# Performance work log

Measured on AMD Instinct MI355X. Metric: run time of the kernel, lower is better.

## Reference

```python
import jax, jax.numpy as jnp
import numpy as np

LN_EPS = 1e-5
NEG_SLOPE = 0.2
INF = float((1 << 32) - 1)


def _ln(x, g, b):
    m = x.mean(-1, keepdims=True)
    v = ((x - m) ** 2).mean(-1, keepdims=True)
    return (x - m) * jax.lax.rsqrt(v + LN_EPS) * g + b


def setup_inputs() -> dict:
    B, M, NPG = 128, 256, 192      # graphs, max nodes per graph, actual nodes per graph
    N = B * NPG                    # 24576 total nodes
    E = N * 16                     # 393216 edges (avg degree 16)
    d, H, Od = 256, 4, 64          # input/attn dim, heads, per-head dim
    out_dim = 256
    key = jax.random.key(0)
    ks = jax.random.split(key, 24)
    s = 0.05
    p = lambda k, sh: jax.random.normal(k, sh, jnp.float32) * s

    node_feat = jax.random.normal(ks[0], (N, d), jnp.float32)
    edge_feat = jax.random.normal(ks[1], (E, d), jnp.float32)
    edge_index = jax.random.randint(ks[2], (2, E), 0, N)
    ptr = jnp.arange(B + 1, dtype=jnp.int32) * NPG
    row_valid = jnp.arange(M) < NPG
    attn_mask = jnp.broadcast_to(row_valid[None, :, None] & row_valid[None, None, :], (B, M, M))

    return dict(
        node_feat=node_feat, attn_mask=attn_mask, edge_feat=edge_feat,
        edge_index=edge_index, num_nodes=N, ptr=ptr,
        Wq=p(ks[3], (d, H * Od)), Wk=p(ks[4], (d, H * Od)), Wv=p(ks[5], (d, H * Od)),
        alphaQ=p(ks[6], (H, Od)), alphaK=p(ks[7], (H, Od)), attn_bias=p(ks[8], (H, Od)),
        gin_eps=jnp.zeros((), jnp.float32),
        gin_W1=p(ks[9], (d, 2 * d)), gin_b1=jnp.zeros((2 * d,), jnp.float32),
        gin_W2=p(ks[10], (2 * d, d)), gin_b2=jnp.zeros((d,), jnp.float32),
        ln1_g=jnp.ones((d,), jnp.float32), ln1_b=jnp.zeros((d,), jnp.float32),
        ln2_g=jnp.ones((d,), jnp.float32), ln2_b=jnp.zeros((d,), jnp.float32),
        ff_W1=p(ks[11], (2 * d, out_dim)), ff_b1=jnp.zeros((out_dim,), jnp.float32),
        ff_W2=p(ks[12], (out_dim, out_dim)), ff_b2=jnp.zeros((out_dim,), jnp.float32),
    )


def reference(node_feat, attn_mask, edge_feat, edge_index, num_nodes, ptr,
              Wq, Wk, Wv, alphaQ, alphaK, attn_bias,
              gin_eps, gin_W1, gin_b1, gin_W2, gin_b2,
              ln1_g, ln1_b, ln2_g, ln2_b,
              ff_W1, ff_b1, ff_W2, ff_b2):
    B, M = attn_mask.shape[:2]
    N, d = node_feat.shape
    H = alphaQ.shape[0]

    # graph -> dense batch layout (scatter by (graph, local position))
    node_ids = jnp.arange(N)
    batch_id = jnp.searchsorted(ptr, node_ids, side='right') - 1
    local = node_ids - ptr[batch_id]
    attn_input = jnp.zeros((B, M, d), node_feat.dtype).at[batch_id, local].set(node_feat)

    # GAT-style additive multi-head attention
    Qp = (attn_input @ Wq).reshape(B, M, H, -1)
    Kp = (attn_input @ Wk).reshape(B, M, H, -1)
    Vp = (attn_input @ Wv).reshape(B, M, H, -1)
    aQ = jnp.einsum('bmhd,hd->bmh', Qp, alphaQ)
    aK = jnp.einsum('bmhd,hd->bmh', Kp, alphaK)
    w = jax.nn.leaky_relu(aQ[:, :, None, :] + aK[:, None, :, :], NEG_SLOPE)  # [B,Q,K,H]
    w = jnp.where(attn_mask[..., None], w, -INF)
    w = jax.nn.softmax(w, axis=2)
    attn_out = (jnp.einsum('bqkh,bkhd->bqhd', w, Vp) + attn_bias).reshape(B, M, -1)

    attn_res = _ln(attn_out + attn_input, ln1_g, ln1_b)[batch_id, local]  # back to [N, d]

    # GIN conv: relu(x[dst] + e) scatter-summed to src, then 2-layer MLP
    msg = jax.nn.relu(node_feat[edge_index[1]] + edge_feat)
    agg = jax.ops.segment_sum(msg, edge_index[0], num_segments=num_nodes)
    h = (1.0 + gin_eps) * node_feat + agg
    gin = jax.nn.relu(h @ gin_W1 + gin_b1) @ gin_W2 + gin_b2
    gin_res = _ln(gin + node_feat, ln2_g, ln2_b)

    x = jnp.concatenate([gin_res, attn_res], axis=-1)  # [N, 2d]
    return jax.nn.relu(x @ ff_W1 + ff_b1) @ ff_W2 + ff_b2
```

## Files before the change

### kernel.cpp

```cpp
#include <hip/hip_runtime.h>

#define LN_EPS 1e-5f
#define NEG_SLOPE 0.2f

typedef __attribute__((ext_vector_type(8))) short short8;
typedef __attribute__((ext_vector_type(4))) float f32x4;

__device__ __forceinline__ unsigned short f2bf(float f) {
  union { float f; unsigned int u; } v;
  v.f = f;
  unsigned int r = v.u + 0x7fffu + ((v.u >> 16) & 1u);
  return (unsigned short)(r >> 16);
}
__device__ __forceinline__ float bf2f(unsigned short u) {
  union { unsigned int u; float f; } v;
  v.u = ((unsigned int)u) << 16;
  return v.f;
}

__device__ __forceinline__ void gld_lds16(const void* g, void* l) {
  __builtin_amdgcn_global_load_lds(
      (const __attribute__((address_space(1))) unsigned int*)g,
      (__attribute__((address_space(3))) unsigned int*)l, 16, 0, 0);
}

template <bool RELU, bool BIAS, bool OUTBF>
__device__ __forceinline__ void gemm_role(
    int t, char* smemc, const unsigned short* __restrict__ A,
    const unsigned short* __restrict__ Bt, const float* __restrict__ bias,
    void* __restrict__ Cv, int N, int K) {
  uint4* As = (uint4*)smemc;
  uint4* Bs = (uint4*)smemc + 512;
  const int tid = threadIdx.x;
  const int wid = tid >> 6, lane = tid & 63;
  const int nC = N >> 7;
  const int row0 = (t / nC) << 6;
  const int col0 = (t % nC) << 7;
  const int wr = wid >> 1, wc = wid & 1;
  const int fr = lane & 15, fq = lane >> 4;

  f32x4 acc[2][4];
#pragma unroll
  for (int m = 0; m < 2; ++m)
#pragma unroll
    for (int n = 0; n < 4; ++n) acc[m][n] = (f32x4){0.f, 0.f, 0.f, 0.f};

  for (int k0 = 0; k0 < K; k0 += 64) {
    __syncthreads();
#pragma unroll
    for (int c = 0; c < 2; ++c) {
      int idx = c * 256 + tid;
      int row = idx >> 3, gs = (idx & 7) ^ (row & 7);
      gld_lds16(A + (size_t)(row0 + row) * K + k0 + gs * 8, As + (idx & ~63));
    }
#pragma unroll
    for (int c = 0; c < 4; ++c) {
      int idx = c * 256 + tid;
      int row = idx >> 3, gs = (idx & 7) ^ (row & 7);
      gld_lds16(Bt + (size_t)(col0 + row) * K + k0 + gs * 8, Bs + (idx & ~63));
    }
    __syncthreads();
#pragma unroll
    for (int kk = 0; kk < 2; ++kk) {
      short8 af[2], bfr[4];
#pragma unroll
      for (int m = 0; m < 2; ++m) {
        int row = wr * 32 + m * 16 + fr;
        af[m] = *(const short8*)&As[row * 8 + ((kk * 4 + fq) ^ (row & 7))];
      }
#pragma unroll
      for (int n = 0; n < 4; ++n) {
        int col = wc * 64 + n * 16 + fr;
        bfr[n] = *(const short8*)&Bs[col * 8 + ((kk * 4 + fq) ^ (col & 7))];
      }
#pragma unroll
      for (int m = 0; m < 2; ++m)
#pragma unroll
        for (int n = 0; n < 4; ++n)
          acc[m][n] = __builtin_amdgcn_mfma_f32_16x16x32_bf16(af[m], bfr[n],
                                                              acc[m][n], 0, 0, 0);
    }
  }

#pragma unroll
  for (int n = 0; n < 4; ++n) {
    const int col = col0 + wc * 64 + n * 16 + fr;
    const float bv = BIAS ? bias[col] : 0.f;
#pragma unroll
    for (int m = 0; m < 2; ++m) {
#pragma unroll
      for (int r = 0; r < 4; ++r) {
        int row = row0 + wr * 32 + m * 16 + fq * 4 + r;
        float v = acc[m][n][r];
        if (BIAS) v += bv;
        if (RELU) v = fmaxf(v, 0.f);
        if (OUTBF)
          ((unsigned short*)Cv)[(size_t)row * N + col] = f2bf(v);
        else
          ((float*)Cv)[(size_t)row * N + col] = v;
      }
    }
  }
}

__device__ __forceinline__ void gather_role(
    int t, const float* __restrict__ node, const unsigned short* __restrict__ nf16,
    const float* __restrict__ ef, const int2* __restrict__ edges,
    const int* __restrict__ ofs, const float* __restrict__ eps_p,
    unsigned short* __restrict__ agg16) {
  const int n = t * 4 + (threadIdx.x >> 6);
  const int lane = threadIdx.x & 63;
  const int s0 = ofs[n];
  const int s1 = ofs[n + 1];
  const float epl = 1.f + eps_p[0];
  const f32x4* nodev = (const f32x4*)node;
  const f32x4* efv = (const f32x4*)ef;
  const ushort4* nfv = (const ushort4*)nf16;
  f32x4 xv = nodev[(size_t)n * 64 + lane];
  float a0 = epl * xv.x, a1 = epl * xv.y, a2 = epl * xv.z, a3 = epl * xv.w;
  int j = s0;
  for (; j + 4 <= s1; j += 4) {
    int2 ed0 = edges[j], ed1 = edges[j + 1], ed2 = edges[j + 2],
         ed3 = edges[j + 3];
    f32x4 e0 = __builtin_nontemporal_load(&efv[(size_t)ed0.x * 64 + lane]);
    f32x4 e1 = __builtin_nontemporal_load(&efv[(size_t)ed1.x * 64 + lane]);
    f32x4 e2 = __builtin_nontemporal_load(&efv[(size_t)ed2.x * 64 + lane]);
    f32x4 e3 = __builtin_nontemporal_load(&efv[(size_t)ed3.x * 64 + lane]);
    ushort4 m0 = nfv[(size_t)ed0.y * 64 + lane];
    ushort4 m1 = nfv[(size_t)ed1.y * 64 + lane];
    ushort4 m2 = nfv[(size_t)ed2.y * 64 + lane];
    ushort4 m3 = nfv[(size_t)ed3.y * 64 + lane];
    a0 += fmaxf(e0.x + bf2f(m0.x), 0.f) + fmaxf(e1.x + bf2f(m1.x), 0.f) +
          fmaxf(e2.x + bf2f(m2.x), 0.f) + fmaxf(e3.x + bf2f(m3.x), 0.f);
    a1 += fmaxf(e0.y + bf2f(m0.y), 0.f) + fmaxf(e1.y + bf2f(m1.y), 0.f) +
          fmaxf(e2.y + bf2f(m2.y), 0.f) + fmaxf(e3.y + bf2f(m3.y), 0.f);
    a2 += fmaxf(e0.z + bf2f(m0.z), 0.f) + fmaxf(e1.z + bf2f(m1.z), 0.f) +
          fmaxf(e2.z + bf2f(m2.z), 0.f) + fmaxf(e3.z + bf2f(m3.z), 0.f);
    a3 += fmaxf(e0.w + bf2f(m0.w), 0.f) + fmaxf(e1.w + bf2f(m1.w), 0.f) +
          fmaxf(e2.w + bf2f(m2.w), 0.f) + fmaxf(e3.w + bf2f(m3.w), 0.f);
  }
  for (; j < s1; ++j) {
    int2 ed = edges[j];
    f32x4 ev = __builtin_nontemporal_load(&efv[(size_t)ed.x * 64 + lane]);
    ushort4 mv = nfv[(size_t)ed.y * 64 + lane];
    a0 += fmaxf(ev.x + bf2f(mv.x), 0.f);
    a1 += fmaxf(ev.y + bf2f(mv.y), 0.f);
    a2 += fmaxf(ev.z + bf2f(mv.z), 0.f);
    a3 += fmaxf(ev.w + bf2f(mv.w), 0.f);
  }
  ushort4 o;
  o.x = f2bf(a0);
  o.y = f2bf(a1);
  o.z = f2bf(a2);
  o.w = f2bf(a3);
  *(ushort4*)(agg16 + (size_t)n * 256 + lane * 4) = o;
}

__device__ __forceinline__ void attn_role(
    int t, char* smemc, const float* __restrict__ aQ,
    const float* __restrict__ aK, const unsigned short* __restrict__ Vp16,
    const float* __restrict__ attn_bias, const int* __restrict__ ptr,
    unsigned short* __restrict__ attn16) {
  unsigned short* Vt = (unsigned short*)smemc;
  float* aQs = (float*)(smemc + 24576);
  float* aKs = aQs + 192;
  float* sinv = aKs + 192;
  float* kmax_s = sinv + 192;
  const int b = t >> 2, h = t & 3;
  const int n0 = ptr[b];
  const int tid = threadIdx.x;
  const int wid = tid >> 6, lane = tid & 63;

  if (tid < 192) {
    aQs[tid] = aQ[(size_t)(n0 + tid) * 4 + h];
    aKs[tid] = aK[(size_t)(n0 + tid) * 4 + h];
  }
  for (int i = tid; i < 1536; i += 256) {
    int k = i >> 3, cc = (i & 7) << 3;
    short8 v = *(const short8*)(Vp16 + (size_t)(n0 + k) * 256 + h * 64 + cc);
    int ks = k >> 3, kr = k & 7;
#pragma unroll
    for (int jj = 0; jj < 8; ++jj) {
      int c = cc + jj;
      Vt[c * 192 + ((ks ^ (c & 7)) << 3) + kr] = (unsigned short)v[jj];
    }
  }
  __syncthreads();
  if (wid == 0) {
    float m3 = fmaxf(fmaxf(aKs[lane], aKs[lane + 64]), aKs[lane + 128]);
#pragma unroll
    for (int off = 32; off; off >>= 1) m3 = fmaxf(m3, __shfl_xor(m3, off));
    if (lane == 0) kmax_s[0] = m3;
  }
  __syncthreads();
  const float kmax = kmax_s[0];
  const int fr = lane & 15, fq = lane >> 4;
  const int qbase = wid * 48;

  float aq_m[3], mm[3];
#pragma unroll
  for (int m = 0; m < 3; ++m) {
    float aqv = aQs[qbase + m * 16 + fr];
    aq_m[m] = aqv;
    float tt = aqv + kmax;
    mm[m] = tt > 0.f ? tt : NEG_SLOPE * tt;
  }

  f32x4 acc[3][4];
#pragma unroll
  for (int m = 0; m < 3; ++m)
#pragma unroll
    for (int n = 0; n < 4; ++n) acc[m][n] = (f32x4){0.f, 0.f, 0.f, 0.f};
  float psum[3] = {0.f, 0.f, 0.f};

  for (int ks = 0; ks < 6; ++ks) {
    short8 bf[4];
#pragma unroll
    for (int n = 0; n < 4; ++n) {
      int c = n * 16 + fr;
      bf[n] = *(const short8*)&Vt[c * 192 + ((((ks << 2) + fq) ^ (c & 7)) << 3)];
    }
    float ak[8];
#pragma unroll
    for (int j = 0; j < 8; ++j) ak[j] = aKs[(ks << 5) + (fq << 3) + j];
#pragma unroll
    for (int m = 0; m < 3; ++m) {
      short8 af;
      float ps = 0.f;
#pragma unroll
      for (int j = 0; j < 8; ++j) {
        float x = aq_m[m] + ak[j];
        x = x > 0.f ? x : NEG_SLOPE * x;
        float p = __expf(x - mm[m]);
        ps += p;
        af[j] = (short)f2bf(p);
      }
      psum[m] += ps;
#pragma unroll
      for (int n = 0; n < 4; ++n)
        acc[m][n] =
            __builtin_amdgcn_mfma_f32_16x16x32_bf16(af, bf[n], acc[m][n], 0, 0, 0);
    }
  }

#pragma unroll
  for (int m = 0; m < 3; ++m) {
    psum[m] += __shfl_xor(psum[m], 16);
    psum[m] += __shfl_xor(psum[m], 32);
  }
  if (fq == 0) {
#pragma unroll
    for (int m = 0; m < 3; ++m) sinv[qbase + m * 16 + fr] = 1.f / psum[m];
  }
  __syncthreads();

#pragma unroll
  for (int m = 0; m < 3; ++m) {
#pragma unroll
    for (int n = 0; n < 4; ++n) {
      int col = n * 16 + fr;
      float bv = attn_bias[h * 64 + col];
#pragma unroll
      for (int r = 0; r < 4; ++r) {
        int q = qbase + m * 16 + fq * 4 + r;
        float v = acc[m][n][r] * sinv[q] + bv;
        attn16[(size_t)(n0 + q) * 256 + h * 64 + col] = f2bf(v);
      }
    }
  }
}

__device__ __forceinline__ void fc2ln_role(
    int t, char* smemc, const unsigned short* __restrict__ A,
    const unsigned short* __restrict__ Bt, const float* __restrict__ b2,
    const float* __restrict__ res, const float* __restrict__ g,
    const float* __restrict__ bln, unsigned short* __restrict__ x2) {
  uint4* As = (uint4*)smemc;
  uint4* Bs = (uint4*)smemc + 512;
  float2* part = (float2*)((uint4*)smemc + 2560);
  const int tid = threadIdx.x;
  const int wid = tid >> 6, lane = tid & 63;
  const int row0 = t << 6;
  const int wr = wid >> 2, wc = wid & 3;
  const int fr = lane & 15, fq = lane >> 4;
  const int K = 512;

  f32x4 acc[2][4];
#pragma unroll
  for (int m = 0; m < 2; ++m)
#pragma unroll
    for (int n = 0; n < 4; ++n) acc[m][n] = (f32x4){0.f, 0.f, 0.f, 0.f};

  for (int k0 = 0; k0 < K; k0 += 64) {
    __syncthreads();
    {
      int row = tid >> 3, gs = (tid & 7) ^ (row & 7);
      gld_lds16(A + (size_t)(row0 + row) * K + k0 + gs * 8, As + (tid & ~63));
    }
#pragma unroll
    for (int c = 0; c < 4; ++c) {
      int idx = c * 512 + tid;
      int row = idx >> 3, gs = (idx & 7) ^ (row & 7);
      gld_lds16(Bt + (size_t)row * K + k0 + gs * 8, Bs + (idx & ~63));
    }
    __syncthreads();
#pragma unroll
    for (int kk = 0; kk < 2; ++kk) {
      short8 af[2], bfr[4];
#pragma unroll
      for (int m = 0; m < 2; ++m) {
        int row = wr * 32 + m * 16 + fr;
        af[m] = *(const short8*)&As[row * 8 + ((kk * 4 + fq) ^ (row & 7))];
      }
#pragma unroll
      for (int n = 0; n < 4; ++n) {
        int col = wc * 64 + n * 16 + fr;
        bfr[n] = *(const short8*)&Bs[col * 8 + ((kk * 4 + fq) ^ (col & 7))];
      }
#pragma unroll
      for (int m = 0; m < 2; ++m)
#pragma unroll
        for (int n = 0; n < 4; ++n)
          acc[m][n] = __builtin_amdgcn_mfma_f32_16x16x32_bf16(af[m], bfr[n],
                                                              acc[m][n], 0, 0, 0);
    }
  }

  float psum[2][4], psq[2][4];
#pragma unroll
  for (int m = 0; m < 2; ++m)
#pragma unroll
    for (int r = 0; r < 4; ++r) {
      psum[m][r] = 0.f;
      psq[m][r] = 0.f;
    }
#pragma unroll
  for (int n = 0; n < 4; ++n) {
    const int col = wc * 64 + n * 16 + fr;
    const float bv = b2[col];
#pragma unroll
    for (int m = 0; m < 2; ++m) {
#pragma unroll
      for (int r = 0; r < 4; ++r) {
        int row = row0 + wr * 32 + m * 16 + fq * 4 + r;
        float v = acc[m][n][r] + bv + res[(size_t)row * 256 + col];
        acc[m][n][r] = v;
        psum[m][r] += v;
        psq[m][r] += v * v;
      }
    }
  }
#pragma unroll
  for (int off = 1; off < 16; off <<= 1) {
#pragma unroll
    for (int m = 0; m < 2; ++m)
#pragma unroll
      for (int r = 0; r < 4; ++r) {
        psum[m][r] += __shfl_xor(psum[m][r], off);
        psq[m][r] += __shfl_xor(psq[m][r], off);
      }
  }
  if (fr == 0) {
#pragma unroll
    for (int m = 0; m < 2; ++m)
#pragma unroll
      for (int r = 0; r < 4; ++r)
        part[(wr * 32 + m * 16 + fq * 4 + r) * 4 + wc] =
            make_float2(psum[m][r], psq[m][r]);
  }
  __syncthreads();

#pragma unroll
  for (int m = 0; m < 2; ++m) {
#pragma unroll
    for (int r = 0; r < 4; ++r) {
      const int lr = wr * 32 + m * 16 + fq * 4 + r;
      float2 p0 = part[lr * 4 + 0], p1 = part[lr * 4 + 1],
             p2 = part[lr * 4 + 2], p3 = part[lr * 4 + 3];
      const float mean = (p0.x + p1.x + p2.x + p3.x) * (1.f / 256.f);
      const float var =
          (p0.y + p1.y + p2.y + p3.y) * (1.f / 256.f) - mean * mean;
      const float rs = rsqrtf(var + LN_EPS);
      const int row = row0 + lr;
#pragma unroll
      for (int n = 0; n < 4; ++n) {
        const int col = wc * 64 + n * 16 + fr;
        float v = (acc[m][n][r] - mean) * rs * g[col] + bln[col];
        x2[(size_t)row * 512 + col] = f2bf(v);
      }
    }
  }
}

__device__ __forceinline__ void ln1_role(
    int t, const unsigned short* __restrict__ xin,
    const float* __restrict__ res, const float* __restrict__ g,
    const float* __restrict__ bt, unsigned short* __restrict__ out) {
  const int n = t * 8 + (threadIdx.x >> 6);
  const int lane = threadIdx.x & 63;
  ushort4 xv = *(const ushort4*)(xin + (size_t)n * 256 + lane * 4);
  float v0 = bf2f(xv.x), v1 = bf2f(xv.y), v2 = bf2f(xv.z), v3 = bf2f(xv.w);
  float4 rv = *(const float4*)(res + (size_t)n * 256 + lane * 4);
  v0 += rv.x;
  v1 += rv.y;
  v2 += rv.z;
  v3 += rv.w;
  float s = v0 + v1 + v2 + v3;
  float ss = v0 * v0 + v1 * v1 + v2 * v2 + v3 * v3;
#pragma unroll
  for (int off = 32; off; off >>= 1) {
    s += __shfl_xor(s, off);
    ss += __shfl_xor(ss, off);
  }
  const float mean = s * (1.f / 256.f);
  const float var = ss * (1.f / 256.f) - mean * mean;
  const float rs = rsqrtf(var + LN_EPS);
  float4 gv = *(const float4*)(g + lane * 4);
  float4 bv = *(const float4*)(bt + lane * 4);
  ushort4 o;
  o.x = f2bf((v0 - mean) * rs * gv.x + bv.x);
  o.y = f2bf((v1 - mean) * rs * gv.y + bv.y);
  o.z = f2bf((v2 - mean) * rs * gv.z + bv.z);
  o.w = f2bf((v3 - mean) * rs * gv.w + bv.w);
  *(ushort4*)(out + (size_t)n * 512 + 256 + lane * 4) = o;
}

__global__ __launch_bounds__(256) void k_fold(
    const float* __restrict__ Wq, const float* __restrict__ Wk,
    const float* __restrict__ alphaQ, const float* __restrict__ alphaK,
    float* __restrict__ wqa, float* __restrict__ wka, int* __restrict__ ideg,
    int Nn) {
  int t = threadIdx.x;
  for (int i = t; i < Nn; i += 256) ideg[i] = 0;
  for (int h = 0; h < 4; ++h) {
    float sq = 0.f, sk = 0.f;
    for (int od = 0; od < 64; ++od) {
      sq += Wq[t * 256 + h * 64 + od] * alphaQ[h * 64 + od];
      sk += Wk[t * 256 + h * 64 + od] * alphaK[h * 64 + od];
    }
    wqa[t * 4 + h] = sq;
    wka[t * 4 + h] = sk;
  }
}

__global__ __launch_bounds__(256) void k_mega(
    const float* __restrict__ Wv, const float* __restrict__ gW1,
    const float* __restrict__ gW2, const float* __restrict__ fW1,
    const float* __restrict__ fW2, unsigned short* __restrict__ wvt,
    unsigned short* __restrict__ w1t, unsigned short* __restrict__ w2t,
    unsigned short* __restrict__ fw1t, unsigned short* __restrict__ fw2t,
    const int* __restrict__ ei, int* __restrict__ ideg, int E,
    const float* __restrict__ node_feat, unsigned short* __restrict__ nf16,
    const float* __restrict__ wqa, const float* __restrict__ wka,
    float* __restrict__ aQ, float* __restrict__ aK) {
  const int bid = blockIdx.x;
  if (bid < 2048) {
    int i = bid * 256 + threadIdx.x;
    const float* src;
    unsigned short* dst;
    int K, N, base;
    if (i < 65536) {
      src = Wv; dst = wvt; K = 256; N = 256; base = 0;
    } else if (i < 196608) {
      src = gW1; dst = w1t; K = 256; N = 512; base = 65536;
    } else if (i < 327680) {
      src = gW2; dst = w2t; K = 512; N = 256; base = 196608;
    } else if (i < 458752) {
      src = fW1; dst = fw1t; K = 512; N = 256; base = 327680;
    } else {
      src = fW2; dst = fw2t; K = 256; N = 256; base = 458752;
    }
    int j = i - base;
    int n = j / K, k = j - n * K;
    dst[j] = f2bf(src[(size_t)k * N + n]);
    return;
  }
  if (bid < 3584) {
    int e = (bid - 2048) * 256 + threadIdx.x;
    if (e < E) atomicAdd(&ideg[ei[e]], 1);
    return;
  }
  const int n = (bid - 3584) * 4 + (threadIdx.x >> 6);
  const int lane = threadIdx.x & 63;
  f32x4 x = ((const f32x4*)node_feat)[(size_t)n * 64 + lane];
  ushort4 o;
  o.x = f2bf(x.x);
  o.y = f2bf(x.y);
  o.z = f2bf(x.z);
  o.w = f2bf(x.w);
  ((ushort4*)nf16)[(size_t)n * 64 + lane] = o;
  float sq[4], sk[4];
  const int d0 = lane * 4;
#pragma unroll
  for (int h = 0; h < 4; ++h) {
    sq[h] = x.x * wqa[(d0 + 0) * 4 + h] + x.y * wqa[(d0 + 1) * 4 + h] +
            x.z * wqa[(d0 + 2) * 4 + h] + x.w * wqa[(d0 + 3) * 4 + h];
    sk[h] = x.x * wka[(d0 + 0) * 4 + h] + x.y * wka[(d0 + 1) * 4 + h] +
            x.z * wka[(d0 + 2) * 4 + h] + x.w * wka[(d0 + 3) * 4 + h];
  }
#pragma unroll
  for (int off = 32; off; off >>= 1) {
#pragma unroll
    for (int h = 0; h < 4; ++h) {
      sq[h] += __shfl_xor(sq[h], off);
      sk[h] += __shfl_xor(sk[h], off);
    }
  }
  if (lane == 0) {
#pragma unroll
    for (int h = 0; h < 4; ++h) {
      aQ[(size_t)n * 4 + h] = sq[h];
      aK[(size_t)n * 4 + h] = sk[h];
    }
  }
}

__global__ __launch_bounds__(1024) void k_scan(const int* __restrict__ deg,
                                               int* __restrict__ ofs,
                                               int* __restrict__ cursor,
                                               int Nn) {
  __shared__ int part[1024];
  const int t = threadIdx.x;
  const int CH = (Nn + 1023) / 1024;
  const int base = t * CH;
  int s = 0;
  for (int i = 0; i < CH; ++i) s += (base + i < Nn) ? deg[base + i] : 0;
  part[t] = s;
  __syncthreads();
  for (int off = 1; off < 1024; off <<= 1) {
    int v = (t >= off) ? part[t - off] : 0;
    __syncthreads();
    part[t] += v;
    __syncthreads();
  }
  int o = (t == 0) ? 0 : part[t - 1];
  for (int i = 0; i < CH; ++i) {
    if (base + i < Nn) {
      ofs[base + i] = o;
      cursor[base + i] = o;
      o += deg[base + i];
    }
  }
  if (t == 1023) ofs[Nn] = part[1023];
}

__global__ __launch_bounds__(256) void k_scatter(const int* __restrict__ ei,
                                                 int* __restrict__ cursor,
                                                 int2* __restrict__ edges,
                                                 int E) {
  int e = blockIdx.x * 256 + threadIdx.x;
  if (e < E) {
    int src = ei[e];
    int dst = ei[E + e];
    int pos = atomicAdd(&cursor[src], 1);
    edges[pos] = make_int2(e, dst);
  }
}

__global__ __launch_bounds__(256) void k_gv(
    int nbV, const unsigned short* __restrict__ nf16,
    const unsigned short* __restrict__ wvt, unsigned short* __restrict__ vp16,
    const float* __restrict__ node, const float* __restrict__ ef,
    const int2* __restrict__ edges, const int* __restrict__ ofs,
    const float* __restrict__ eps_p, unsigned short* __restrict__ agg16) {
  __shared__ __align__(16) char smem[24576];
  if ((int)blockIdx.x < nbV)
    gemm_role<false, false, true>(blockIdx.x, smem, nf16, wvt, nullptr, vp16,
                                  256, 256);
  else
    gather_role(blockIdx.x - nbV, node, nf16, ef, edges, ofs, eps_p, agg16);
}

__global__ __launch_bounds__(256) void k_fa(
    int nbA, const float* __restrict__ aQ, const float* __restrict__ aK,
    const unsigned short* __restrict__ vp16,
    const float* __restrict__ attn_bias, const int* __restrict__ ptr,
    unsigned short* __restrict__ at16, const unsigned short* __restrict__ agg16,
    const unsigned short* __restrict__ w1t, const float* __restrict__ gin_b1,
    unsigned short* __restrict__ t1_16) {
  __shared__ __align__(16) char smem[26944];
  if ((int)blockIdx.x < nbA)
    attn_role(blockIdx.x, smem, aQ, aK, vp16, attn_bias, ptr, at16);
  else
    gemm_role<true, true, true>(blockIdx.x - nbA, smem, agg16, w1t, gin_b1,
                                t1_16, 512, 256);
}

__global__ __launch_bounds__(512) void k_f2l(
    int nbG, const unsigned short* __restrict__ t1_16,
    const unsigned short* __restrict__ w2t, const float* __restrict__ gin_b2,
    const float* __restrict__ node_feat, const float* __restrict__ ln2_g,
    const float* __restrict__ ln2_b, const unsigned short* __restrict__ at16,
    const float* __restrict__ ln1_g, const float* __restrict__ ln1_b,
    unsigned short* __restrict__ x2_16) {
  __shared__ __align__(16) char smem[43520];
  if ((int)blockIdx.x < nbG)
    fc2ln_role(blockIdx.x, smem, t1_16, w2t, gin_b2, node_feat, ln2_g, ln2_b,
               x2_16);
  else
    ln1_role(blockIdx.x - nbG, at16, node_feat, ln1_g, ln1_b, x2_16);
}

template <bool RELU, bool BIAS, bool OUTBF>
__global__ __launch_bounds__(256) void k_gemm(
    const unsigned short* __restrict__ A, const unsigned short* __restrict__ Bt,
    const float* __restrict__ bias, void* __restrict__ Cv, int N, int K) {
  __shared__ __align__(16) char smem[24576];
  gemm_role<RELU, BIAS, OUTBF>(blockIdx.x, smem, A, Bt, bias, Cv, N, K);
}

extern "C" void kernel_launch(void* const* d_in, const int* in_sizes, int n_in,
                              void* d_out, int out_size, void* d_ws,
                              size_t ws_size, hipStream_t stream) {
  const float* node_feat = (const float*)d_in[0];
  const float* edge_feat = (const float*)d_in[2];
  const int* edge_index = (const int*)d_in[3];
  const int* ptr = (const int*)d_in[5];
  const float* Wq = (const float*)d_in[6];
  const float* Wk = (const float*)d_in[7];
  const float* Wv = (const float*)d_in[8];
  const float* alphaQ = (const float*)d_in[9];
  const float* alphaK = (const float*)d_in[10];
  const float* attn_bias = (const float*)d_in[11];
  const float* gin_eps = (const float*)d_in[12];
  const float* gin_W1 = (const float*)d_in[13];
  const float* gin_b1 = (const float*)d_in[14];
  const float* gin_W2 = (const float*)d_in[15];
  const float* gin_b2 = (const float*)d_in[16];
  const float* ln1_g = (const float*)d_in[17];
  const float* ln1_b = (const float*)d_in[18];
  const float* ln2_g = (const float*)d_in[19];
  const float* ln2_b = (const float*)d_in[20];
  const float* ff_W1 = (const float*)d_in[21];
  const float* ff_b1 = (const float*)d_in[22];
  const float* ff_W2 = (const float*)d_in[23];
  const float* ff_b2 = (const float*)d_in[24];

  const int N = in_sizes[0] / 256;
  const int E = in_sizes[2] / 256;
  const int B = in_sizes[5] - 1;

  float* ws = (float*)d_ws;
  float* buf0 = ws;
  unsigned short* x2_16 = (unsigned short*)(buf0 + (size_t)N * 256);
  unsigned short* agg16 = x2_16 + (size_t)N * 512;
  unsigned short* t1_16 = agg16 + (size_t)N * 256;
  unsigned short* h1_16 = t1_16 + (size_t)N * 512;
  unsigned short* nf16 = h1_16 + (size_t)N * 256;
  unsigned short* vp16 = nf16 + (size_t)N * 256;
  unsigned short* at16 = vp16 + (size_t)N * 256;
  unsigned short* wvt = at16 + (size_t)N * 256;
  unsigned short* w1t = wvt + 65536;
  unsigned short* w2t = w1t + 131072;
  unsigned short* ffw1t = w2t + 131072;
  unsigned short* ffw2t = ffw1t + 131072;
  float* wqa = (float*)(ffw2t + 65536);
  float* wka = wqa + 1024;
  float* aQ = wka + 1024;
  float* aK = aQ + (size_t)N * 4;
  int* ideg = (int*)(aK + (size_t)N * 4);
  int* ofs = ideg + N;
  int* cursor = ofs + N + 2;
  int2* edges = (int2*)(cursor + N);
  size_t need = (size_t)N * 256 * 4 + (size_t)N * 2304 * 2 + 1100000 +
                (size_t)N * 8 * 4 + (size_t)N * 16 + (size_t)E * 8 + 8192;
  if (ws_size < need) return;

  const int degB = (E + 255) / 256;

  k_fold<<<1, 256, 0, stream>>>(Wq, Wk, alphaQ, alphaK, wqa, wka, ideg, N);
  k_mega<<<2048 + degB + N / 4, 256, 0, stream>>>(
      Wv, gin_W1, gin_W2, ff_W1, ff_W2, wvt, w1t, w2t, ffw1t, ffw2t,
      edge_index, ideg, E, node_feat, nf16, wqa, wka, aQ, aK);

  k_scan<<<1, 1024, 0, stream>>>(ideg, ofs, cursor, N);
  k_scatter<<<degB, 256, 0, stream>>>(edge_index, cursor, edges, E);

  const int nbV = (N / 64) * 2;
  k_gv<<<nbV + N / 4, 256, 0, stream>>>(nbV, nf16, wvt, vp16, node_feat,
                                        edge_feat, edges, ofs, gin_eps, agg16);

  const int nbA = B * 4;
  k_fa<<<nbA + (N / 64) * 4, 256, 0, stream>>>(nbA, aQ, aK, vp16, attn_bias,
                                               ptr, at16, agg16, w1t, gin_b1,
                                               t1_16);

  const int nbG = N / 64;
  k_f2l<<<nbG + N / 8, 512, 0, stream>>>(nbG, t1_16, w2t, gin_b2, node_feat,
                                         ln2_g, ln2_b, at16, ln1_g, ln1_b,
                                         x2_16);

  k_gemm<true, true, true><<<(N / 64) * 2, 256, 0, stream>>>(x2_16, ffw1t,
                                                             ff_b1, h1_16, 256,
                                                             512);
  k_gemm<false, true, false><<<(N / 64) * 2, 256, 0, stream>>>(
      h1_16, ffw2t, ff_b2, d_out, 256, 256);
}
```

Before: 306.2 us.

## Fuse the two feed-forward GEMMs into one kernel with the hidden tile kept in LDS

Replaces the two separate FF GEMM launches with a single kernel. Each 64-row block computes relu(x@W1+b1) into LDS as bf16, then multiplies that tile by W2 straight away. This removes the global write and re-read of the h1 intermediate and one kernel launch. In exchange there are fewer blocks (N/64 instead of 2x that), each block computes the full 256-wide output, and W2 fragments are read directly from global memory without LDS staging.

After: 308.5 us. No clear change (+0.7%).

```diff
diff --git a/kernel.cpp b/kernel.cpp
--- a/kernel.cpp
+++ b/kernel.cpp
@@ -425,6 +425,127 @@
   *(ushort4*)(out + (size_t)n * 512 + 256 + lane * 4) = o;
 }
 
+__global__ __launch_bounds__(512) void k_ff(
+    const unsigned short* __restrict__ x2, const unsigned short* __restrict__ w1t,
+    const float* __restrict__ b1, const unsigned short* __restrict__ w2t,
+    const float* __restrict__ b2, float* __restrict__ out) {
+  __shared__ __align__(16) char smem[40960];
+  uint4* As = (uint4*)smem;
+  uint4* Bs = (uint4*)smem + 512;
+  uint4* H = (uint4*)smem + 512;
+  unsigned short* H16 = (unsigned short*)H;
+  const int tid = threadIdx.x;
+  const int wid = tid >> 6, lane = tid & 63;
+  const int row0 = blockIdx.x << 6;
+  const int wr = wid >> 2, wc = wid & 3;
+  const int fr = lane & 15, fq = lane >> 4;
+
+  f32x4 acc[2][4];
+#pragma unroll
+  for (int m = 0; m < 2; ++m)
+#pragma unroll
+    for (int n = 0; n < 4; ++n) acc[m][n] = (f32x4){0.f, 0.f, 0.f, 0.f};
+
+  for (int k0 = 0; k0 < 512; k0 += 64) {
+    __syncthreads();
+    {
+      int row = tid >> 3, gs = (tid & 7) ^ (row & 7);
+      gld_lds16(x2 + (size_t)(row0 + row) * 512 + k0 + gs * 8, As + (tid & ~63));
+    }
+#pragma unroll
+    for (int c = 0; c < 4; ++c) {
+      int idx = c * 512 + tid;
+      int row = idx >> 3, gs = (idx & 7) ^ (row & 7);
+      gld_lds16(w1t + (size_t)row * 512 + k0 + gs * 8, Bs + (idx & ~63));
+    }
+    __syncthreads();
+#pragma unroll
+    for (int kk = 0; kk < 2; ++kk) {
+      short8 af[2], bfr[4];
+#pragma unroll
+      for (int m = 0; m < 2; ++m) {
+        int row = wr * 32 + m * 16 + fr;
+        af[m] = *(const short8*)&As[row * 8 + ((kk * 4 + fq) ^ (row & 7))];
+      }
+#pragma unroll
+      for (int n = 0; n < 4; ++n) {
+        int col = wc * 64 + n * 16 + fr;
+        bfr[n] = *(const short8*)&Bs[col * 8 + ((kk * 4 + fq) ^ (col & 7))];
+      }
+#pragma unroll
+      for (int m = 0; m < 2; ++m)
+#pragma unroll
+        for (int n = 0; n < 4; ++n)
+          acc[m][n] = __builtin_amdgcn_mfma_f32_16x16x32_bf16(af[m], bfr[n],
+                                                              acc[m][n], 0, 0, 0);
+    }
+  }
+
+  __syncthreads();
+#pragma unroll
+  for (int n = 0; n < 4; ++n) {
+    const int col = wc * 64 + n * 16 + fr;
+    const int s = col >> 3, e = col & 7;
+    const float bv = b1[col];
+#pragma unroll
+    for (int m = 0; m < 2; ++m) {
+#pragma unroll
+      for (int r = 0; r < 4; ++r) {
+        int row = wr * 32 + m * 16 + fq * 4 + r;
+        float v = fmaxf(acc[m][n][r] + bv, 0.f);
+        int sw = (s & ~7) | ((s & 7) ^ (row & 7));
+        H16[row * 256 + sw * 8 + e] = f2bf(v);
+      }
+    }
+  }
+  __syncthreads();
+
+  f32x4 acc2[2][4];
+#pragma unroll
+  for (int m = 0; m < 2; ++m)
+#pragma unroll
+    for (int n = 0; n < 4; ++n) acc2[m][n] = (f32x4){0.f, 0.f, 0.f, 0.f};
+
+#pragma unroll
+  for (int t2 = 0; t2 < 4; ++t2) {
+#pragma unroll
+    for (int kk = 0; kk < 2; ++kk) {
+      short8 af[2], bfr[4];
+#pragma unroll
+      for (int m = 0; m < 2; ++m) {
+        int row = wr * 32 + m * 16 + fr;
+        af[m] = *(const short8*)&H[row * 32 + t2 * 8 + ((kk * 4 + fq) ^ (row & 7))];
+      }
+#pragma unroll
+      for (int n = 0; n < 4; ++n) {
+        int col = wc * 64 + n * 16 + fr;
+        bfr[n] = *(const short8*)(w2t + (size_t)col * 256 + t2 * 64 +
+                                  (kk * 4 + fq) * 8);
+      }
+#pragma unroll
+      for (int m = 0; m < 2; ++m)
+#pragma unroll
+        for (int n = 0; n < 4; ++n)
+          acc2[m][n] = __builtin_amdgcn_mfma_f32_16x16x32_bf16(af[m], bfr[n],
+                                                               acc2[m][n], 0, 0, 0);
+    }
+  }
+
+#pragma unroll
+  for (int n = 0; n < 4; ++n) {
+    const int col = wc * 64 + n * 16 + fr;
+    const float bv = b2[col];
+#pragma unroll
+    for (int m = 0; m < 2; ++m) {
+#pragma unroll
+      for (int r = 0; r < 4; ++r) {
+        int row = row0 + wr * 32 + m * 16 + fq * 4 + r;
+        out[(size_t)row * 256 + col] = acc2[m][n][r] + bv;
+      }
+    }
+  }
+}
+
 __global__ __launch_bounds__(256) void k_fold(
     const float* __restrict__ Wq, const float* __restrict__ Wk,
     const float* __restrict__ alphaQ, const float* __restrict__ alphaK,
@@ -601,14 +722,6 @@
     ln1_role(blockIdx.x - nbG, at16, node_feat, ln1_g, ln1_b, x2_16);
 }
 
-template <bool RELU, bool BIAS, bool OUTBF>
-__global__ __launch_bounds__(256) void k_gemm(
-    const unsigned short* __restrict__ A, const unsigned short* __restrict__ Bt,
-    const float* __restrict__ bias, void* __restrict__ Cv, int N, int K) {
-  __shared__ __align__(16) char smem[24576];
-  gemm_role<RELU, BIAS, OUTBF>(blockIdx.x, smem, A, Bt, bias, Cv, N, K);
-}
-
 extern "C" void kernel_launch(void* const* d_in, const int* in_sizes, int n_in,
                               void* d_out, int out_size, void* d_ws,
                               size_t ws_size, hipStream_t stream) {
@@ -690,9 +803,6 @@
                                          ln2_g, ln2_b, at16, ln1_g, ln1_b,
                                          x2_16);
 
-  k_gemm<true, true, true><<<(N / 64) * 2, 256, 0, stream>>>(x2_16, ffw1t,
-                                                             ff_b1, h1_16, 256,
-                                                             512);
-  k_gemm<false, true, false><<<(N / 64) * 2, 256, 0, stream>>>(
-      h1_16, ffw2t, ff_b2, d_out, 256, 256);
-}
+  k_ff<<<N / 64, 512, 0, stream>>>(x2_16, ffw1t, ff_b1, ffw2t, ff_b2,
+                                   (float*)d_out);
+}
```
